# Optimization experiments

Measured on AMD Instinct MI355X. Metric: run time of the kernel, lower is better.

The kernel has to match this reference:

```python
import jax, jax.numpy as jnp
import numpy as np

N = 50000
E = 1600000
IN, OUT = 128, 64


def _gcn(h, W, b, src, dst):
    # DGL GraphConv, norm='both', weight applied first (in>out), activation=relu
    x = h @ W  # [N, OUT]
    ones = jnp.ones((src.shape[0],), dtype=h.dtype)
    deg_out = jnp.clip(jax.ops.segment_sum(ones, src, num_segments=N), 1.0)
    deg_in = jnp.clip(jax.ops.segment_sum(ones, dst, num_segments=N), 1.0)
    x = x * jax.lax.rsqrt(deg_out)[:, None]
    agg = jax.ops.segment_sum(x[src], dst, num_segments=N)  # SpMM
    agg = agg * jax.lax.rsqrt(deg_in)[:, None]
    return jax.nn.relu(agg + b)


def setup_inputs() -> dict:
    key = jax.random.key(0)
    ks = jax.random.split(key, 10)
    inp = {"h": jax.random.normal(ks[0], (N, IN), dtype=jnp.float32)}
    for i in range(3):
        inp[f"src{i}"] = jax.random.randint(ks[1 + 2 * i], (E,), 0, N, dtype=jnp.int32)
        inp[f"dst{i}"] = jax.random.randint(ks[2 + 2 * i], (E,), 0, N, dtype=jnp.int32)
        inp[f"W{i}"] = jax.random.normal(ks[7 + i], (IN, OUT), dtype=jnp.float32) * (1.0 / np.sqrt(IN))
        inp[f"b{i}"] = jnp.zeros((OUT,), dtype=jnp.float32)
    return inp


def reference(h, src0, dst0, src1, dst1, src2, dst2, W0, b0, W1, b1, W2, b2):
    e0 = _gcn(h, W0, b0, src0, dst0)
    e1 = _gcn(h, W1, b1, src1, dst1)
    e2 = _gcn(h, W2, b2, src2, dst2)
    # stack over meta-path dim then mean == average of semantic embeddings
    return (e0 + e1 + e2) / 3.0
```

## Files before the change

kernel.cpp:

```cpp
#include <hip/hip_runtime.h>

#define KDIM 128
#define NCOLS 64
#define NHCH 64
#define HW 12500
#define COARSE 512
#define NC 98
#define SFCAP 17408
#define BUCKET 64
#define NBUCK 782
#define FCAP 2816
#define NPB 85
#define PREP_HIST (3 * NHCH)
#define PREP_CNT  (3 * NPB)
#define PREP_WF   12
#define PREP_CONV 565
#define PREP_GRID (PREP_HIST + PREP_CNT + PREP_WF + PREP_CONV)

typedef __attribute__((ext_vector_type(8))) short bf16x8;
typedef __attribute__((ext_vector_type(4))) float f32x4;

struct GArgs {
  const int*   src[3];
  const int*   dst[3];
  const float* W[3];
  const float* b[3];
  int          E[3];
};

__device__ __forceinline__ unsigned short f2bf(float f) {
  unsigned u = __float_as_uint(f);
  u += 0x7FFFu + ((u >> 16) & 1u);
  return (unsigned short)(u >> 16);
}
__device__ __forceinline__ float bflo(unsigned u) { return __uint_as_float(u << 16); }
__device__ __forceinline__ float bfhi(unsigned u) { return __uint_as_float(u & 0xFFFF0000u); }

__global__ __launch_bounds__(256) void prep_kernel(
    GArgs A, const float* __restrict__ h, unsigned short* __restrict__ hb,
    unsigned short* __restrict__ Wf, unsigned* __restrict__ P8,
    int* __restrict__ tot, int total8) {
  __shared__ unsigned sbuf[HW];
  const int b = blockIdx.x;
  const int t = threadIdx.x;

  if (b < PREP_HIST) {
    const int g = b >> 6;
    const int chunk = b & 63;
    const int E = A.E[g];
    const int per_chunk = (((E + NHCH - 1) / NHCH) + 3) & ~3;
    const int* __restrict__ keys = A.src[g];
    for (int i = t; i < HW; i += 256) sbuf[i] = 0;
    __syncthreads();
    const int e0 = chunk * per_chunk;
    const int e1 = min(e0 + per_chunk, E);
    const int nn = max(e1 - e0, 0);
    const int nv = nn >> 2;
    const int4* k4p = (const int4*)&keys[e0];
    for (int v = t; v < nv; v += 256) {
      int4 k = k4p[v];
      atomicAdd(&sbuf[(unsigned)k.x >> 2], 1u << (((unsigned)k.x & 3u) * 8));
      atomicAdd(&sbuf[(unsigned)k.y >> 2], 1u << (((unsigned)k.y & 3u) * 8));
      atomicAdd(&sbuf[(unsigned)k.z >> 2], 1u << (((unsigned)k.z & 3u) * 8));
      atomicAdd(&sbuf[(unsigned)k.w >> 2], 1u << (((unsigned)k.w & 3u) * 8));
    }
    for (int e = e0 + (nv << 2) + t; e < e1; e += 256) {
      unsigned k = (unsigned)keys[e];
      atomicAdd(&sbuf[k >> 2], 1u << ((k & 3u) * 8));
    }
    __syncthreads();
    unsigned* __restrict__ dstp = P8 + (size_t)b * HW;
    for (int i = t; i < HW; i += 256) dstp[i] = sbuf[i];

  } else if (b < PREP_HIST + PREP_CNT) {
    const int bb = b - PREP_HIST;
    const int g = bb / NPB;
    const int blk = bb % NPB;
    const int E = A.E[g];
    const int per_block = (((E + NPB - 1) / NPB) + 3) & ~3;
    const int* __restrict__ dst = A.dst[g];
    int* hcnt = (int*)sbuf;
    if (t < NC) hcnt[t] = 0;
    __syncthreads();
    const int e0 = blk * per_block;
    const int e1 = min(e0 + per_block, E);
    const int nn = max(e1 - e0, 0);
    const int nv = nn >> 2;
    const int4* d4 = (const int4*)&dst[e0];
    for (int v = t; v < nv; v += 256) {
      int4 d = d4[v];
      atomicAdd(&hcnt[(unsigned)d.x >> 9], 1);
      atomicAdd(&hcnt[(unsigned)d.y >> 9], 1);
      atomicAdd(&hcnt[(unsigned)d.z >> 9], 1);
      atomicAdd(&hcnt[(unsigned)d.w >> 9], 1);
    }
    for (int e = e0 + (nv << 2) + t; e < e1; e += 256)
      atomicAdd(&hcnt[(unsigned)dst[e] >> 9], 1);
    __syncthreads();
    if (t < NC && hcnt[t]) atomicAdd(&tot[g * NC + t], hcnt[t]);

  } else if (b < PREP_HIST + PREP_CNT + PREP_WF) {
    int tid = (b - PREP_HIST - PREP_CNT) * 256 + t;
    int lane = tid & 63;
    int frag = (tid >> 6) & 15;
    int g = tid >> 10;
    int c = frag >> 2, kk = frag & 3;
    int n = lane & 15, quad = lane >> 4;
    const float* W = A.W[g];
    unsigned short v[8];
    #pragma unroll
    for (int j = 0; j < 8; ++j) {
      int k = 32 * kk + quad * 8 + j;
      v[j] = f2bf(W[k * 64 + 4 * n + c]);
    }
    uint4 u;
    u.x = (unsigned)v[0] | ((unsigned)v[1] << 16);
    u.y = (unsigned)v[2] | ((unsigned)v[3] << 16);
    u.z = (unsigned)v[4] | ((unsigned)v[5] << 16);
    u.w = (unsigned)v[6] | ((unsigned)v[7] << 16);
    ((uint4*)Wf)[tid] = u;

  } else {
    const int cb = b - (PREP_HIST + PREP_CNT + PREP_WF);
    for (int i = cb * 256 + t; i < total8; i += PREP_CONV * 256) {
      const float4* hp = (const float4*)(h + (size_t)i * 8);
      float4 f0 = hp[0];
      float4 f1 = hp[1];
      uint4 u;
      u.x = (unsigned)f2bf(f0.x) | ((unsigned)f2bf(f0.y) << 16);
      u.y = (unsigned)f2bf(f0.z) | ((unsigned)f2bf(f0.w) << 16);
      u.z = (unsigned)f2bf(f1.x) | ((unsigned)f2bf(f1.y) << 16);
      u.w = (unsigned)f2bf(f1.z) | ((unsigned)f2bf(f1.w) << 16);
      ((uint4*)hb)[i] = u;
    }
  }
}

__global__ __launch_bounds__(128) void scan_off_kernel(
    const int* __restrict__ tot, int* __restrict__ off, int* __restrict__ cursor) {
  __shared__ int sd[128];
  const int t = threadIdx.x;
  for (int g = 0; g < 3; ++g) {
    int v = (t < NC) ? tot[g * NC + t] : 0;
    sd[t] = v;
    __syncthreads();
    for (int o = 1; o < 128; o <<= 1) {
      int add = (t >= o) ? sd[t - o] : 0;
      __syncthreads();
      sd[t] += add;
      __syncthreads();
    }
    int excl = sd[t] - v;
    if (t < NC) { off[g * (NC + 1) + t] = excl; cursor[g * NC + t] = excl; }
    if (t == 0) off[g * (NC + 1) + NC] = sd[127];
    __syncthreads();
  }
}

__global__ __launch_bounds__(256) void partition_coarse_kernel(
    GArgs A, int* __restrict__ cursor, unsigned* __restrict__ P2c, int Emax) {
  __shared__ int lcnt[NC];
  __shared__ int lcur[NC];
  const int g = blockIdx.y;
  const int E = A.E[g];
  const int per_block = (((E + NPB - 1) / NPB) + 3) & ~3;
  const int* __restrict__ src = A.src[g];
  const int* __restrict__ dst = A.dst[g];
  unsigned* __restrict__ P2g = P2c + (size_t)g * Emax;
  const int t = threadIdx.x;
  if (t < NC) lcnt[t] = 0;
  __syncthreads();
  const int e0 = blockIdx.x * per_block;
  const int e1 = min(e0 + per_block, E);
  const int n = max(e1 - e0, 0);
  const int nv = n >> 2;
  const int4* d4 = (const int4*)&dst[e0];
  const int4* s4 = (const int4*)&src[e0];
  for (int v = t; v < nv; v += 256) {
    int4 d = d4[v];
    atomicAdd(&lcnt[(unsigned)d.x >> 9], 1);
    atomicAdd(&lcnt[(unsigned)d.y >> 9], 1);
    atomicAdd(&lcnt[(unsigned)d.z >> 9], 1);
    atomicAdd(&lcnt[(unsigned)d.w >> 9], 1);
  }
  for (int e = e0 + (nv << 2) + t; e < e1; e += 256)
    atomicAdd(&lcnt[(unsigned)dst[e] >> 9], 1);
  __syncthreads();
  if (t < NC) {
    int c = lcnt[t];
    lcur[t] = c ? atomicAdd(&cursor[g * NC + t], c) : 0;
  }
  __syncthreads();
  for (int v = t; v < nv; v += 256) {
    int4 d = d4[v];
    int4 s = s4[v];
    unsigned bk; int pos;
    bk = (unsigned)d.x >> 9; pos = atomicAdd(&lcur[bk], 1);
    P2g[pos] = (unsigned)s.x | (((unsigned)d.x & 511u) << 16);
    bk = (unsigned)d.y >> 9; pos = atomicAdd(&lcur[bk], 1);
    P2g[pos] = (unsigned)s.y | (((unsigned)d.y & 511u) << 16);
    bk = (unsigned)d.z >> 9; pos = atomicAdd(&lcur[bk], 1);
    P2g[pos] = (unsigned)s.z | (((unsigned)d.z & 511u) << 16);
    bk = (unsigned)d.w >> 9; pos = atomicAdd(&lcur[bk], 1);
    P2g[pos] = (unsigned)s.w | (((unsigned)d.w & 511u) << 16);
  }
  for (int e = e0 + (nv << 2) + t; e < e1; e += 256) {
    unsigned d = (unsigned)dst[e];
    unsigned bk = d >> 9;
    int pos = atomicAdd(&lcur[bk], 1);
    P2g[pos] = (unsigned)src[e] | ((d & 511u) << 16);
  }
}

__global__ __launch_bounds__(512) void sort_fine_kernel(
    const unsigned* __restrict__ P2c, const int* __restrict__ off,
    unsigned short* __restrict__ S, int* __restrict__ row_start,
    int N, int Emax) {
  __shared__ int cnt[COARSE];
  __shared__ int sd[COARSE];
  __shared__ int cur[COARSE];
  __shared__ unsigned short outl[SFCAP];
  const int c = blockIdx.x;
  const int g = blockIdx.y;
  const unsigned* __restrict__ P2g = P2c + (size_t)g * Emax;
  const int base_e = off[g * (NC + 1) + c];
  const int nloc = off[g * (NC + 1) + c + 1] - base_e;
  const int t = threadIdx.x;

  cnt[t] = 0;
  __syncthreads();
  for (int i = t; i < nloc; i += 512)
    atomicAdd(&cnt[(P2g[base_e + i] >> 16) & 511u], 1);
  __syncthreads();
  int v = cnt[t];
  sd[t] = v;
  __syncthreads();
  for (int o = 1; o < 512; o <<= 1) {
    int add = (t >= o) ? sd[t - o] : 0;
    __syncthreads();
    sd[t] += add;
    __syncthreads();
  }
  int excl = sd[t] - v;
  cur[t] = excl;
  int node = c * COARSE + t;
  if (node <= N) row_start[g * (N + 1) + node] = base_e + excl;
  __syncthreads();
  for (int i = t; i < nloc; i += 512) {
    unsigned p = P2g[base_e + i];
    int pos = atomicAdd(&cur[(p >> 16) & 511u], 1);
    if (pos < SFCAP) outl[pos] = (unsigned short)(p & 0xFFFFu);
  }
  __syncthreads();
  unsigned short* __restrict__ Sg = S + (size_t)g * Emax;
  for (int i = t; i < nloc; i += 512) Sg[base_e + i] = outl[i];
}

__global__ __launch_bounds__(512) void gemm_mfma_kernel(
    GArgs A, const unsigned short* __restrict__ hb,
    const unsigned short* __restrict__ Wf, const unsigned* __restrict__ P8,
    unsigned short* __restrict__ x, int N) {
  __shared__ unsigned ldegw[64];
  const int g = blockIdx.y;
  unsigned short* __restrict__ xg = x + (size_t)g * N * NCOLS;
  const int t = threadIdx.x;
  const int row0 = blockIdx.x * 128;

  if (t < 64) ldegw[t] = 0;
  __syncthreads();
  if (t < 256) {
    const unsigned* __restrict__ Pg = P8 + (size_t)g * NHCH * HW;
    const int widx = t >> 3;
    const int cg = t & 7;
    const int wcol = min((row0 >> 2) + widx, HW - 1);
    unsigned lo = 0, hi = 0;
    #pragma unroll
    for (int cc = 0; cc < 8; ++cc) {
      unsigned wv = Pg[(size_t)(cg * 8 + cc) * HW + wcol];
      lo += wv & 0x00FF00FFu;
      hi += (wv >> 8) & 0x00FF00FFu;
    }
    atomicAdd(&ldegw[2 * widx], lo);
    atomicAdd(&ldegw[2 * widx + 1], hi);
  }

  const int lane = t & 63;
  const int w = t >> 6;
  const int quad = lane >> 4;
  const int n = lane & 15;

  int arow = min(row0 + w * 16 + n, N - 1);
  const unsigned short* hrow = hb + (size_t)arow * KDIM + quad * 8;
  bf16x8 a0 = *(const bf16x8*)(hrow);
  bf16x8 a1 = *(const bf16x8*)(hrow + 32);
  bf16x8 a2 = *(const bf16x8*)(hrow + 64);
  bf16x8 a3 = *(const bf16x8*)(hrow + 96);

  const uint4* wfp = (const uint4*)Wf + (size_t)g * 1024 + lane;

  f32x4 acc[4];
  #pragma unroll
  for (int c = 0; c < 4; ++c) acc[c] = (f32x4)(0.f);

  __syncthreads();

  #pragma unroll
  for (int c = 0; c < 4; ++c) {
    union { uint4 u; bf16x8 v; } b0, b1, b2, b3;
    b0.u = wfp[(size_t)(c * 4 + 0) * 64];
    b1.u = wfp[(size_t)(c * 4 + 1) * 64];
    b2.u = wfp[(size_t)(c * 4 + 2) * 64];
    b3.u = wfp[(size_t)(c * 4 + 3) * 64];
    acc[c] = __builtin_amdgcn_mfma_f32_16x16x32_bf16(a0, b0.v, acc[c], 0, 0, 0);
    acc[c] = __builtin_amdgcn_mfma_f32_16x16x32_bf16(a1, b1.v, acc[c], 0, 0, 0);
    acc[c] = __builtin_amdgcn_mfma_f32_16x16x32_bf16(a2, b2.v, acc[c], 0, 0, 0);
    acc[c] = __builtin_amdgcn_mfma_f32_16x16x32_bf16(a3, b3.v, acc[c], 0, 0, 0);
  }

  const int rbase = row0 + w * 16 + quad * 4;
  #pragma unroll
  for (int r = 0; r < 4; ++r) {
    int row = rbase + r;
    if (row < N) {
      int lr = row - row0;
      float dg = (float)((ldegw[2 * (lr >> 2) + (lr & 1)] >> (((lr >> 1) & 1) * 16)) & 0xFFFFu);
      float s = rsqrtf(fmaxf(dg, 1.0f));
      uint2 o;
      o.x = (unsigned)f2bf(acc[0][r] * s) | ((unsigned)f2bf(acc[1][r] * s) << 16);
      o.y = (unsigned)f2bf(acc[2][r] * s) | ((unsigned)f2bf(acc[3][r] * s) << 16);
      *(uint2*)(xg + (size_t)row * NCOLS + 4 * n) = o;
    }
  }
}

__global__ __launch_bounds__(512) void spmm_all_kernel(
    GArgs A, const unsigned short* __restrict__ S,
    const int* __restrict__ row_start, const unsigned short* __restrict__ x,
    float* __restrict__ out, int N, int Emax) {
  __shared__ int rs[BUCKET + 1];
  __shared__ unsigned short srcs[FCAP];

  const int t = threadIdx.x;
  const int bk = blockIdx.x;
  const int dbase = bk * BUCKET;
  const int nd = min(BUCKET, N - dbase);
  const int grp = t >> 3;
  const int qe = (t & 7) * 8;

  float tot[8];
  #pragma unroll
  for (int j = 0; j < 8; ++j) tot[j] = 0.f;

  for (int g = 0; g < 3; ++g) {
    const unsigned short* __restrict__ Sg = S + (size_t)g * Emax;
    const int* __restrict__ rsg = row_start + (size_t)g * (N + 1);
    const unsigned short* __restrict__ xg = x + (size_t)g * N * NCOLS;

    __syncthreads();
    if (t <= BUCKET) rs[t] = rsg[min(dbase + t, N)];
    __syncthreads();
    const int e0 = rs[0];
    const int ne = min(rs[BUCKET] - e0, FCAP);
    for (int i = t; i < ne; i += 512) srcs[i] = Sg[e0 + i];
    __syncthreads();

    if (grp < nd) {
      int i = rs[grp] - e0;
      const int iend = min(rs[grp + 1] - e0, ne);
      const int deg = iend - i;
      float acc[8];
      #pragma unroll
      for (int j = 0; j < 8; ++j) acc[j] = 0.f;
      for (; i + 3 < iend; i += 4) {
        int sa = srcs[i + 0];
        int sb = srcs[i + 1];
        int sc = srcs[i + 2];
        int sdd = srcs[i + 3];
        uint4 ua = *(const uint4*)&xg[(size_t)sa * NCOLS + qe];
        uint4 ub = *(const uint4*)&xg[(size_t)sb * NCOLS + qe];
        uint4 uc = *(const uint4*)&xg[(size_t)sc * NCOLS + qe];
        uint4 ud = *(const uint4*)&xg[(size_t)sdd * NCOLS + qe];
        acc[0] += bflo(ua.x) + bflo(ub.x) + bflo(uc.x) + bflo(ud.x);
        acc[1] += bfhi(ua.x) + bfhi(ub.x) + bfhi(uc.x) + bfhi(ud.x);
        acc[2] += bflo(ua.y) + bflo(ub.y) + bflo(uc.y) + bflo(ud.y);
        acc[3] += bfhi(ua.y) + bfhi(ub.y) + bfhi(uc.y) + bfhi(ud.y);
        acc[4] += bflo(ua.z) + bflo(ub.z) + bflo(uc.z) + bflo(ud.z);
        acc[5] += bfhi(ua.z) + bfhi(ub.z) + bfhi(uc.z) + bfhi(ud.z);
        acc[6] += bflo(ua.w) + bflo(ub.w) + bflo(uc.w) + bflo(ud.w);
        acc[7] += bfhi(ua.w) + bfhi(ub.w) + bfhi(uc.w) + bfhi(ud.w);
      }
      for (; i < iend; ++i) {
        int s = srcs[i];
        uint4 u = *(const uint4*)&xg[(size_t)s * NCOLS + qe];
        acc[0] += bflo(u.x); acc[1] += bfhi(u.x);
        acc[2] += bflo(u.y); acc[3] += bfhi(u.y);
        acc[4] += bflo(u.z); acc[5] += bfhi(u.z);
        acc[6] += bflo(u.w); acc[7] += bfhi(u.w);
      }
      float sc2 = rsqrtf(fmaxf((float)deg, 1.0f));
      const float* bg = A.b[g] + qe;
      #pragma unroll
      for (int j = 0; j < 8; ++j)
        tot[j] += fmaxf(fmaf(acc[j], sc2, bg[j]), 0.f) * (1.0f / 3.0f);
    }
  }

  if (grp < nd) {
    float* op = &out[(size_t)(dbase + grp) * NCOLS + qe];
    *(float4*)&op[0] = make_float4(tot[0], tot[1], tot[2], tot[3]);
    *(float4*)&op[4] = make_float4(tot[4], tot[5], tot[6], tot[7]);
  }
}

extern "C" void kernel_launch(void* const* d_in, const int* in_sizes, int n_in,
                              void* d_out, int out_size, void* d_ws, size_t ws_size,
                              hipStream_t stream) {
  const float* h = (const float*)d_in[0];
  const int N = in_sizes[0] / KDIM;
  float* out = (float*)d_out;

  GArgs A;
  int Emax = 0;
  for (int g = 0; g < 3; ++g) {
    A.src[g] = (const int*)  d_in[1 + g * 4];
    A.dst[g] = (const int*)  d_in[2 + g * 4];
    A.W[g]   = (const float*)d_in[3 + g * 4];
    A.b[g]   = (const float*)d_in[4 + g * 4];
    A.E[g]   = in_sizes[1 + g * 4];
    if (A.E[g] > Emax) Emax = A.E[g];
  }

  char* w = (char*)d_ws;
  unsigned short* x = (unsigned short*)w;
  char* w2 = w + (size_t)3 * N * NCOLS * sizeof(unsigned short);
  unsigned short* hb = (unsigned short*)w2;
  char* w3 = w2 + (size_t)N * KDIM * sizeof(unsigned short);
  unsigned* P2c = (unsigned*)w3;
  char* w4 = w3 + (size_t)3 * Emax * sizeof(unsigned);
  unsigned* P8 = (unsigned*)w4;
  char* w5 = w4 + (size_t)3 * NHCH * HW * sizeof(unsigned);
  unsigned short* S = (unsigned short*)w5;
  char* w6 = w5 + (size_t)3 * Emax * sizeof(unsigned short);
  unsigned short* Wf = (unsigned short*)w6;
  char* w7 = w6 + (size_t)3 * 16 * 64 * 8 * sizeof(unsigned short);
  int* row_start = (int*)w7;
  char* w8 = w7 + (size_t)3 * (N + 1) * sizeof(int);
  int* tot    = (int*)w8;
  int* off    = tot + 3 * NC;
  int* cursor = off + 3 * (NC + 1);

  hipMemsetAsync(tot, 0, 3 * NC * sizeof(int), stream);
  const int total8 = N * KDIM / 8;
  prep_kernel<<<PREP_GRID, 256, 0, stream>>>(A, h, hb, Wf, P8, tot, total8);
  scan_off_kernel<<<1, 128, 0, stream>>>(tot, off, cursor);
  partition_coarse_kernel<<<dim3(NPB, 3), 256, 0, stream>>>(A, cursor, P2c, Emax);
  sort_fine_kernel<<<dim3(NC, 3), 512, 0, stream>>>(P2c, off, S, row_start, N, Emax);
  gemm_mfma_kernel<<<dim3((N + 127) / 128, 3), 512, 0, stream>>>(A, hb, Wf, P8, x, N);
  spmm_all_kernel<<<NBUCK, 512, 0, stream>>>(A, S, row_start, x, out, N, Emax);
}
```

Before: 268.7 us.

## Replace two-level bucket sort with global-atomic degree counting and direct scatter

Drops the shared-memory packed histograms and the coarse-partition plus fine-sort pipeline. Per-node in and out degrees are now counted with global atomics, row_start comes from a per-chunk scan, and edges are scattered straight into CSR with global atomic cursors. That scatter is fused into one launch with the MFMA GEMM so the two can overlap. This removes several launches and passes over the edge data, at the cost of heavy contended global atomics and a nondeterministic order of edges within each row.

```diff
diff --git a/kernel.cpp b/kernel.cpp
--- a/kernel.cpp
+++ b/kernel.cpp
@@ -2,20 +2,18 @@
 
 #define KDIM 128
 #define NCOLS 64
-#define NHCH 64
-#define HW 12500
-#define COARSE 512
-#define NC 98
-#define SFCAP 17408
 #define BUCKET 64
 #define NBUCK 782
 #define FCAP 2816
 #define NPB 85
-#define PREP_HIST (3 * NHCH)
-#define PREP_CNT  (3 * NPB)
-#define PREP_WF   12
-#define PREP_CONV 565
-#define PREP_GRID (PREP_HIST + PREP_CNT + PREP_WF + PREP_CONV)
+#define PREP_DEG (3 * NPB)
+#define PREP_WF  12
+#define PREP_CONV 757
+#define PREP_GRID (PREP_DEG + PREP_WF + PREP_CONV)
+#define PG_SCAT (3 * NPB)
+#define PG_GEMM_PER 391
+#define PG_GEMM (3 * PG_GEMM_PER)
+#define PG_GRID (PG_SCAT + PG_GEMM)
 
 typedef __attribute__((ext_vector_type(8))) short bf16x8;
 typedef __attribute__((ext_vector_type(4))) float f32x4;
@@ -38,69 +36,41 @@
 
 __global__ __launch_bounds__(256) void prep_kernel(
     GArgs A, const float* __restrict__ h, unsigned short* __restrict__ hb,
-    unsigned short* __restrict__ Wf, unsigned* __restrict__ P8,
-    int* __restrict__ tot, int total8) {
-  __shared__ unsigned sbuf[HW];
+    unsigned short* __restrict__ Wf, int* __restrict__ deg_out,
+    int* __restrict__ deg_in, int N, int total8) {
   const int b = blockIdx.x;
   const int t = threadIdx.x;
 
-  if (b < PREP_HIST) {
-    const int g = b >> 6;
-    const int chunk = b & 63;
-    const int E = A.E[g];
-    const int per_chunk = (((E + NHCH - 1) / NHCH) + 3) & ~3;
-    const int* __restrict__ keys = A.src[g];
-    for (int i = t; i < HW; i += 256) sbuf[i] = 0;
-    __syncthreads();
-    const int e0 = chunk * per_chunk;
-    const int e1 = min(e0 + per_chunk, E);
-    const int nn = max(e1 - e0, 0);
-    const int nv = nn >> 2;
-    const int4* k4p = (const int4*)&keys[e0];
-    for (int v = t; v < nv; v += 256) {
-      int4 k = k4p[v];
-      atomicAdd(&sbuf[(unsigned)k.x >> 2], 1u << (((unsigned)k.x & 3u) * 8));
-      atomicAdd(&sbuf[(unsigned)k.y >> 2], 1u << (((unsigned)k.y & 3u) * 8));
-      atomicAdd(&sbuf[(unsigned)k.z >> 2], 1u << (((unsigned)k.z & 3u) * 8));
-      atomicAdd(&sbuf[(unsigned)k.w >> 2], 1u << (((unsigned)k.w & 3u) * 8));
-    }
-    for (int e = e0 + (nv << 2) + t; e < e1; e += 256) {
-      unsigned k = (unsigned)keys[e];
-      atomicAdd(&sbuf[k >> 2], 1u << ((k & 3u) * 8));
-    }
-    __syncthreads();
-    unsigned* __restrict__ dstp = P8 + (size_t)b * HW;
-    for (int i = t; i < HW; i += 256) dstp[i] = sbuf[i];
-
-  } else if (b < PREP_HIST + PREP_CNT) {
-    const int bb = b - PREP_HIST;
-    const int g = bb / NPB;
-    const int blk = bb % NPB;
+  if (b < PREP_DEG) {
+    const int g = b / NPB;
+    const int blk = b % NPB;
     const int E = A.E[g];
     const int per_block = (((E + NPB - 1) / NPB) + 3) & ~3;
+    const int* __restrict__ src = A.src[g];
     const int* __restrict__ dst = A.dst[g];
-    int* hcnt = (int*)sbuf;
-    if (t < NC) hcnt[t] = 0;
-    __syncthreads();
+    int* __restrict__ dout = deg_out + (size_t)g * N;
+    int* __restrict__ din  = deg_in  + (size_t)g * N;
     const int e0 = blk * per_block;
     const int e1 = min(e0 + per_block, E);
     const int nn = max(e1 - e0, 0);
     const int nv = nn >> 2;
+    const int4* s4 = (const int4*)&src[e0];
     const int4* d4 = (const int4*)&dst[e0];
     for (int v = t; v < nv; v += 256) {
+      int4 s = s4[v];
       int4 d = d4[v];
-      atomicAdd(&hcnt[(unsigned)d.x >> 9], 1);
-      atomicAdd(&hcnt[(unsigned)d.y >> 9], 1);
-      atomicAdd(&hcnt[(unsigned)d.z >> 9], 1);
-      atomicAdd(&hcnt[(unsigned)d.w >> 9], 1);
-    }
-    for (int e = e0 + (nv << 2) + t; e < e1; e += 256)
-      atomicAdd(&hcnt[(unsigned)dst[e] >> 9], 1);
-    __syncthreads();
-    if (t < NC && hcnt[t]) atomicAdd(&tot[g * NC + t], hcnt[t]);
-
-  } else if (b < PREP_HIST + PREP_CNT + PREP_WF) {
-    int tid = (b - PREP_HIST - PREP_CNT) * 256 + t;
+      atomicAdd(&dout[s.x], 1); atomicAdd(&dout[s.y], 1);
+      atomicAdd(&dout[s.z], 1); atomicAdd(&dout[s.w], 1);
+      atomicAdd(&din[d.x], 1);  atomicAdd(&din[d.y], 1);
+      atomicAdd(&din[d.z], 1);  atomicAdd(&din[d.w], 1);
+    }
+    for (int e = e0 + (nv << 2) + t; e < e1; e += 256) {
+      atomicAdd(&dout[src[e]], 1);
+      atomicAdd(&din[dst[e]], 1);
+    }
+
+  } else if (b < PREP_DEG + PREP_WF) {
+    int tid = (b - PREP_DEG) * 256 + t;
     int lane = tid & 63;
     int frag = (tid >> 6) & 15;
     int g = tid >> 10;
@@ -121,7 +91,7 @@
     ((uint4*)Wf)[tid] = u;
 
   } else {
-    const int cb = b - (PREP_HIST + PREP_CNT + PREP_WF);
+    const int cb = b - (PREP_DEG + PREP_WF);
     for (int i = cb * 256 + t; i < total8; i += PREP_CONV * 256) {
       const float4* hp = (const float4*)(h + (size_t)i * 8);
       float4 f0 = hp[0];
@@ -136,103 +106,30 @@
   }
 }
 
-__global__ __launch_bounds__(128) void scan_off_kernel(
-    const int* __restrict__ tot, int* __restrict__ off, int* __restrict__ cursor) {
-  __shared__ int sd[128];
+__global__ __launch_bounds__(512) void scan_rs_kernel(
+    const int* __restrict__ deg_in, int* __restrict__ row_start,
+    int* __restrict__ cursor, int N) {
+  __shared__ int sd[512];
+  __shared__ int sbase;
+  const int g = blockIdx.y;
+  const int c = blockIdx.x;
   const int t = threadIdx.x;
-  for (int g = 0; g < 3; ++g) {
-    int v = (t < NC) ? tot[g * NC + t] : 0;
-    sd[t] = v;
-    __syncthreads();
-    for (int o = 1; o < 128; o <<= 1) {
-      int add = (t >= o) ? sd[t - o] : 0;
-      __syncthreads();
-      sd[t] += add;
-      __syncthreads();
-    }
-    int excl = sd[t] - v;
-    if (t < NC) { off[g * (NC + 1) + t] = excl; cursor[g * NC + t] = excl; }
-    if (t == 0) off[g * (NC + 1) + NC] = sd[127];
-    __syncthreads();
-  }
-}
-
-__global__ __launch_bounds__(256) void partition_coarse_kernel(
-    GArgs A, int* __restrict__ cursor, unsigned* __restrict__ P2c, int Emax) {
-  __shared__ int lcnt[NC];
-  __shared__ int lcur[NC];
-  const int g = blockIdx.y;
-  const int E = A.E[g];
-  const int per_block = (((E + NPB - 1) / NPB) + 3) & ~3;
-  const int* __restrict__ src = A.src[g];
-  const int* __restrict__ dst = A.dst[g];
-  unsigned* __restrict__ P2g = P2c + (size_t)g * Emax;
-  const int t = threadIdx.x;
-  if (t < NC) lcnt[t] = 0;
+  const int* __restrict__ dg = deg_in + (size_t)g * N;
+
+  int acc = 0;
+  const int c512 = c * 512;
+  for (int i = t; i < c512; i += 512) acc += dg[i];
+  sd[t] = acc;
   __syncthreads();
-  const int e0 = blockIdx.x * per_block;
-  const int e1 = min(e0 + per_block, E);
-  const int n = max(e1 - e0, 0);
-  const int nv = n >> 2;
-  const int4* d4 = (const int4*)&dst[e0];
-  const int4* s4 = (const int4*)&src[e0];
-  for (int v = t; v < nv; v += 256) {
-    int4 d = d4[v];
-    atomicAdd(&lcnt[(unsigned)d.x >> 9], 1);
-    atomicAdd(&lcnt[(unsigned)d.y >> 9], 1);
-    atomicAdd(&lcnt[(unsigned)d.z >> 9], 1);
-    atomicAdd(&lcnt[(unsigned)d.w >> 9], 1);
-  }
-  for (int e = e0 + (nv << 2) + t; e < e1; e += 256)
-    atomicAdd(&lcnt[(unsigned)dst[e] >> 9], 1);
+  for (int o = 256; o > 0; o >>= 1) {
+    if (t < o) sd[t] += sd[t + o];
+    __syncthreads();
+  }
+  if (t == 0) sbase = sd[0];
   __syncthreads();
-  if (t < NC) {
-    int c = lcnt[t];
-    lcur[t] = c ? atomicAdd(&cursor[g * NC + t], c) : 0;
-  }
-  __syncthreads();
-  for (int v = t; v < nv; v += 256) {
-    int4 d = d4[v];
-    int4 s = s4[v];
-    unsigned bk; int pos;
-    bk = (unsigned)d.x >> 9; pos = atomicAdd(&lcur[bk], 1);
-    P2g[pos] = (unsigned)s.x | (((unsigned)d.x & 511u) << 16);
-    bk = (unsigned)d.y >> 9; pos = atomicAdd(&lcur[bk], 1);
-    P2g[pos] = (unsigned)s.y | (((unsigned)d.y & 511u) << 16);
-    bk = (unsigned)d.z >> 9; pos = atomicAdd(&lcur[bk], 1);
-    P2g[pos] = (unsigned)s.z | (((unsigned)d.z & 511u) << 16);
-    bk = (unsigned)d.w >> 9; pos = atomicAdd(&lcur[bk], 1);
-    P2g[pos] = (unsigned)s.w | (((unsigned)d.w & 511u) << 16);
-  }
-  for (int e = e0 + (nv << 2) + t; e < e1; e += 256) {
-    unsigned d = (unsigned)dst[e];
-    unsigned bk = d >> 9;
-    int pos = atomicAdd(&lcur[bk], 1);
-    P2g[pos] = (unsigned)src[e] | ((d & 511u) << 16);
-  }
-}
-
-__global__ __launch_bounds__(512) void sort_fine_kernel(
-    const unsigned* __restrict__ P2c, const int* __restrict__ off,
-    unsigned short* __restrict__ S, int* __restrict__ row_start,
-    int N, int Emax) {
-  __shared__ int cnt[COARSE];
-  __shared__ int sd[COARSE];
-  __shared__ int cur[COARSE];
-  __shared__ unsigned short outl[SFCAP];
-  const int c = blockIdx.x;
-  const int g = blockIdx.y;
-  const unsigned* __restrict__ P2g = P2c + (size_t)g * Emax;
-  const int base_e = off[g * (NC + 1) + c];
-  const int nloc = off[g * (NC + 1) + c + 1] - base_e;
-  const int t = threadIdx.x;
-
-  cnt[t] = 0;
-  __syncthreads();
-  for (int i = t; i < nloc; i += 512)
-    atomicAdd(&cnt[(P2g[base_e + i] >> 16) & 511u], 1);
-  __syncthreads();
-  int v = cnt[t];
+
+  const int idx = c512 + t;
+  int v = (idx < N) ? dg[idx] : 0;
   sd[t] = v;
   __syncthreads();
   for (int o = 1; o < 512; o <<= 1) {
@@ -241,94 +138,106 @@
     sd[t] += add;
     __syncthreads();
   }
-  int excl = sd[t] - v;
-  cur[t] = excl;
-  int node = c * COARSE + t;
-  if (node <= N) row_start[g * (N + 1) + node] = base_e + excl;
-  __syncthreads();
-  for (int i = t; i < nloc; i += 512) {
-    unsigned p = P2g[base_e + i];
-    int pos = atomicAdd(&cur[(p >> 16) & 511u], 1);
-    if (pos < SFCAP) outl[pos] = (unsigned short)(p & 0xFFFFu);
-  }
-  __syncthreads();
-  unsigned short* __restrict__ Sg = S + (size_t)g * Emax;
-  for (int i = t; i < nloc; i += 512) Sg[base_e + i] = outl[i];
-}
-
-__global__ __launch_bounds__(512) void gemm_mfma_kernel(
+  int excl = sbase + sd[t] - v;
+  if (idx < N) {
+    row_start[(size_t)g * (N + 1) + idx] = excl;
+    cursor[(size_t)g * N + idx] = excl;
+  } else if (idx == N) {
+    row_start[(size_t)g * (N + 1) + N] = excl;
+  }
+}
+
+__global__ __launch_bounds__(512) void pg_kernel(
     GArgs A, const unsigned short* __restrict__ hb,
-    const unsigned short* __restrict__ Wf, const unsigned* __restrict__ P8,
-    unsigned short* __restrict__ x, int N) {
-  __shared__ unsigned ldegw[64];
-  const int g = blockIdx.y;
-  unsigned short* __restrict__ xg = x + (size_t)g * N * NCOLS;
+    const unsigned short* __restrict__ Wf, const int* __restrict__ deg_out,
+    int* __restrict__ cursor, unsigned short* __restrict__ S,
+    unsigned short* __restrict__ x, int N, int Emax) {
+  const int b = blockIdx.x;
   const int t = threadIdx.x;
-  const int row0 = blockIdx.x * 128;
-
-  if (t < 64) ldegw[t] = 0;
-  __syncthreads();
-  if (t < 256) {
-    const unsigned* __restrict__ Pg = P8 + (size_t)g * NHCH * HW;
-    const int widx = t >> 3;
-    const int cg = t & 7;
-    const int wcol = min((row0 >> 2) + widx, HW - 1);
-    unsigned lo = 0, hi = 0;
+
+  if (b < PG_SCAT) {
+    const int g = b / NPB;
+    const int blk = b % NPB;
+    const int E = A.E[g];
+    const int per_block = (((E + NPB - 1) / NPB) + 3) & ~3;
+    const int* __restrict__ src = A.src[g];
+    const int* __restrict__ dst = A.dst[g];
+    int* __restrict__ cur = cursor + (size_t)g * N;
+    unsigned short* __restrict__ Sg = S + (size_t)g * Emax;
+    const int e0 = blk * per_block;
+    const int e1 = min(e0 + per_block, E);
+    const int nn = max(e1 - e0, 0);
+    const int nv = nn >> 2;
+    const int4* s4 = (const int4*)&src[e0];
+    const int4* d4 = (const int4*)&dst[e0];
+    for (int v = t; v < nv; v += 512) {
+      int4 s = s4[v];
+      int4 d = d4[v];
+      int p0 = atomicAdd(&cur[d.x], 1);
+      int p1 = atomicAdd(&cur[d.y], 1);
+      int p2 = atomicAdd(&cur[d.z], 1);
+      int p3 = atomicAdd(&cur[d.w], 1);
+      Sg[p0] = (unsigned short)s.x;
+      Sg[p1] = (unsigned short)s.y;
+      Sg[p2] = (unsigned short)s.z;
+      Sg[p3] = (unsigned short)s.w;
+    }
+    for (int e = e0 + (nv << 2) + t; e < e1; e += 512) {
+      int p = atomicAdd(&cur[dst[e]], 1);
+      Sg[p] = (unsigned short)src[e];
+    }
+
+  } else {
+    const int gb = b - PG_SCAT;
+    const int g = gb / PG_GEMM_PER;
+    const int blk = gb % PG_GEMM_PER;
+    const int row0 = blk * 128;
+    unsigned short* __restrict__ xg = x + (size_t)g * N * NCOLS;
+    const int* __restrict__ degg = deg_out + (size_t)g * N;
+
+    const int lane = t & 63;
+    const int w = t >> 6;
+    const int quad = lane >> 4;
+    const int n = lane & 15;
+
+    int arow = min(row0 + w * 16 + n, N - 1);
+    const unsigned short* hrow = hb + (size_t)arow * KDIM + quad * 8;
+    bf16x8 a0 = *(const bf16x8*)(hrow);
+    bf16x8 a1 = *(const bf16x8*)(hrow + 32);
+    bf16x8 a2 = *(const bf16x8*)(hrow + 64);
+    bf16x8 a3 = *(const bf16x8*)(hrow + 96);
+
+    const uint4* wfp = (const uint4*)Wf + (size_t)g * 1024 + lane;
+
+    f32x4 acc[4];
     #pragma unroll
-    for (int cc = 0; cc < 8; ++cc) {
-      unsigned wv = Pg[(size_t)(cg * 8 + cc) * HW + wcol];
-      lo += wv & 0x00FF00FFu;
-      hi += (wv >> 8) & 0x00FF00FFu;
-    }
-    atomicAdd(&ldegw[2 * widx], lo);
-    atomicAdd(&ldegw[2 * widx + 1], hi);
-  }
-
-  const int lane = t & 63;
-  const int w = t >> 6;
-  const int quad = lane >> 4;
-  const int n = lane & 15;
-
-  int arow = min(row0 + w * 16 + n, N - 1);
-  const unsigned short* hrow = hb + (size_t)arow * KDIM + quad * 8;
-  bf16x8 a0 = *(const bf16x8*)(hrow);
-  bf16x8 a1 = *(const bf16x8*)(hrow + 32);
-  bf16x8 a2 = *(const bf16x8*)(hrow + 64);
-  bf16x8 a3 = *(const bf16x8*)(hrow + 96);
-
-  const uint4* wfp = (const uint4*)Wf + (size_t)g * 1024 + lane;
-
-  f32x4 acc[4];
-  #pragma unroll
-  for (int c = 0; c < 4; ++c) acc[c] = (f32x4)(0.f);
-
-  __syncthreads();
-
-  #pragma unroll
-  for (int c = 0; c < 4; ++c) {
-    union { uint4 u; bf16x8 v; } b0, b1, b2, b3;
-    b0.u = wfp[(size_t)(c * 4 + 0) * 64];
-    b1.u = wfp[(size_t)(c * 4 + 1) * 64];
-    b2.u = wfp[(size_t)(c * 4 + 2) * 64];
-    b3.u = wfp[(size_t)(c * 4 + 3) * 64];
-    acc[c] = __builtin_amdgcn_mfma_f32_16x16x32_bf16(a0, b0.v, acc[c], 0, 0, 0);
-    acc[c] = __builtin_amdgcn_mfma_f32_16x16x32_bf16(a1, b1.v, acc[c], 0, 0, 0);
-    acc[c] = __builtin_amdgcn_mfma_f32_16x16x32_bf16(a2, b2.v, acc[c], 0, 0, 0);
-    acc[c] = __builtin_amdgcn_mfma_f32_16x16x32_bf16(a3, b3.v, acc[c], 0, 0, 0);
-  }
-
-  const int rbase = row0 + w * 16 + quad * 4;
-  #pragma unroll
-  for (int r = 0; r < 4; ++r) {
-    int row = rbase + r;
-    if (row < N) {
-      int lr = row - row0;
-      float dg = (float)((ldegw[2 * (lr >> 2) + (lr & 1)] >> (((lr >> 1) & 1) * 16)) & 0xFFFFu);
-      float s = rsqrtf(fmaxf(dg, 1.0f));
-      uint2 o;
-      o.x = (unsigned)f2bf(acc[0][r] * s) | ((unsigned)f2bf(acc[1][r] * s) << 16);
-      o.y = (unsigned)f2bf(acc[2][r] * s) | ((unsigned)f2bf(acc[3][r] * s) << 16);
-      *(uint2*)(xg + (size_t)row * NCOLS + 4 * n) = o;
+    for (int c = 0; c < 4; ++c) acc[c] = (f32x4)(0.f);
+
+    #pragma unroll
+    for (int c = 0; c < 4; ++c) {
+      union { uint4 u; bf16x8 v; } b0, b1, b2, b3;
+      b0.u = wfp[(size_t)(c * 4 + 0) * 64];
+      b1.u = wfp[(size_t)(c * 4 + 1) * 64];
+      b2.u = wfp[(size_t)(c * 4 + 2) * 64];
+      b3.u = wfp[(size_t)(c * 4 + 3) * 64];
+      acc[c] = __builtin_amdgcn_mfma_f32_16x16x32_bf16(a0, b0.v, acc[c], 0, 0, 0);
+      acc[c] = __builtin_amdgcn_mfma_f32_16x16x32_bf16(a1, b1.v, acc[c], 0, 0, 0);
+      acc[c] = __builtin_amdgcn_mfma_f32_16x16x32_bf16(a2, b2.v, acc[c], 0, 0, 0);
+      acc[c] = __builtin_amdgcn_mfma_f32_16x16x32_bf16(a3, b3.v, acc[c], 0, 0, 0);
+    }
+
+    const int rbase = row0 + w * 16 + quad * 4;
+    #pragma unroll
+    for (int r = 0; r < 4; ++r) {
+      int row = rbase + r;
+      if (row < N) {
+        float dg = (float)degg[row];
+        float s = rsqrtf(fmaxf(dg, 1.0f));
+        uint2 o;
+        o.x = (unsigned)f2bf(acc[0][r] * s) | ((unsigned)f2bf(acc[1][r] * s) << 16);
+        o.y = (unsigned)f2bf(acc[2][r] * s) | ((unsigned)f2bf(acc[3][r] * s) << 16);
+        *(uint2*)(xg + (size_t)row * NCOLS + 4 * n) = o;
+      }
     }
   }
 }
@@ -435,26 +344,19 @@
   char* w2 = w + (size_t)3 * N * NCOLS * sizeof(unsigned short);
   unsigned short* hb = (unsigned short*)w2;
   char* w3 = w2 + (size_t)N * KDIM * sizeof(unsigned short);
-  unsigned* P2c = (unsigned*)w3;
-  char* w4 = w3 + (size_t)3 * Emax * sizeof(unsigned);
-  unsigned* P8 = (unsigned*)w4;
-  char* w5 = w4 + (size_t)3 * NHCH * HW * sizeof(unsigned);
-  unsigned short* S = (unsigned short*)w5;
-  char* w6 = w5 + (size_t)3 * Emax * sizeof(unsigned short);
-  unsigned short* Wf = (unsigned short*)w6;
-  char* w7 = w6 + (size_t)3 * 16 * 64 * 8 * sizeof(unsigned short);
-  int* row_start = (int*)w7;
-  char* w8 = w7 + (size_t)3 * (N + 1) * sizeof(int);
-  int* tot    = (int*)w8;
-  int* off    = tot + 3 * NC;
-  int* cursor = off + 3 * (NC + 1);
-
-  hipMemsetAsync(tot, 0, 3 * NC * sizeof(int), stream);
+  unsigned short* S = (unsigned short*)w3;
+  char* w4 = w3 + (size_t)3 * Emax * sizeof(unsigned short);
+  unsigned short* Wf = (unsigned short*)w4;
+  char* w5 = w4 + (size_t)3 * 16 * 64 * 8 * sizeof(unsigned short);
+  int* deg_out = (int*)w5;
+  int* deg_in  = deg_out + (size_t)3 * N;
+  int* cursor  = deg_in + (size_t)3 * N;
+  int* row_start = cursor + (size_t)3 * N;
+
+  hipMemsetAsync(deg_out, 0, (size_t)2 * 3 * N * sizeof(int), stream);
   const int total8 = N * KDIM / 8;
-  prep_kernel<<<PREP_GRID, 256, 0, stream>>>(A, h, hb, Wf, P8, tot, total8);
-  scan_off_kernel<<<1, 128, 0, stream>>>(tot, off, cursor);
-  partition_coarse_kernel<<<dim3(NPB, 3), 256, 0, stream>>>(A, cursor, P2c, Emax);
-  sort_fine_kernel<<<dim3(NC, 3), 512, 0, stream>>>(P2c, off, S, row_start, N, Emax);
-  gemm_mfma_kernel<<<dim3((N + 127) / 128, 3), 512, 0, stream>>>(A, hb, Wf, P8, x, N);
+  prep_kernel<<<PREP_GRID, 256, 0, stream>>>(A, h, hb, Wf, deg_out, deg_in, N, total8);
+  scan_rs_kernel<<<dim3(98, 3), 512, 0, stream>>>(deg_in, row_start, cursor, N);
+  pg_kernel<<<PG_GRID, 512, 0, stream>>>(A, hb, Wf, deg_out, cursor, S, x, N, Emax);
   spmm_all_kernel<<<NBUCK, 512, 0, stream>>>(A, S, row_start, x, out, N, Emax);
 }
```

Result: slower. 956.2 us (+255.8%).

## Partition edges directly into 64-node buckets and sort locally inside SpMM

Applied to the files above, without the earlier changes.

Replaces the two-level sort (coarse 512-node partition followed by a separate fine-sort kernel that writes CSR row_start and a compact source array) with a single partition into 782 buckets of 64 destination nodes. Each SpMM block then loads its bucket's packed edges into shared memory, builds a per-node histogram, scans it with a wavefront shuffle and scatters sources locally before aggregating. This removes one kernel launch and one full pass over the edge array, but adds LDS counting-sort work to each SpMM block and uses wider histograms with more global atomics in the prep and partition stages.

```diff
diff --git a/kernel.cpp b/kernel.cpp
--- a/kernel.cpp
+++ b/kernel.cpp
@@ -4,11 +4,8 @@
 #define NCOLS 64
 #define NHCH 64
 #define HW 12500
-#define COARSE 512
-#define NC 98
-#define SFCAP 17408
 #define BUCKET 64
-#define NBUCK 782
+#define NB7 782
 #define FCAP 2816
 #define NPB 85
 #define PREP_HIST (3 * NHCH)
@@ -80,7 +77,7 @@
     const int per_block = (((E + NPB - 1) / NPB) + 3) & ~3;
     const int* __restrict__ dst = A.dst[g];
     int* hcnt = (int*)sbuf;
-    if (t < NC) hcnt[t] = 0;
+    for (int i = t; i < NB7; i += 256) hcnt[i] = 0;
     __syncthreads();
     const int e0 = blk * per_block;
     const int e1 = min(e0 + per_block, E);
@@ -89,15 +86,16 @@
     const int4* d4 = (const int4*)&dst[e0];
     for (int v = t; v < nv; v += 256) {
       int4 d = d4[v];
-      atomicAdd(&hcnt[(unsigned)d.x >> 9], 1);
-      atomicAdd(&hcnt[(unsigned)d.y >> 9], 1);
-      atomicAdd(&hcnt[(unsigned)d.z >> 9], 1);
-      atomicAdd(&hcnt[(unsigned)d.w >> 9], 1);
+      atomicAdd(&hcnt[(unsigned)d.x >> 6], 1);
+      atomicAdd(&hcnt[(unsigned)d.y >> 6], 1);
+      atomicAdd(&hcnt[(unsigned)d.z >> 6], 1);
+      atomicAdd(&hcnt[(unsigned)d.w >> 6], 1);
     }
     for (int e = e0 + (nv << 2) + t; e < e1; e += 256)
-      atomicAdd(&hcnt[(unsigned)dst[e] >> 9], 1);
-    __syncthreads();
-    if (t < NC && hcnt[t]) atomicAdd(&tot[g * NC + t], hcnt[t]);
+      atomicAdd(&hcnt[(unsigned)dst[e] >> 6], 1);
+    __syncthreads();
+    for (int i = t; i < NB7; i += 256)
+      if (hcnt[i]) atomicAdd(&tot[g * NB7 + i], hcnt[i]);
 
   } else if (b < PREP_HIST + PREP_CNT + PREP_WF) {
     int tid = (b - PREP_HIST - PREP_CNT) * 256 + t;
@@ -136,39 +134,46 @@
   }
 }
 
-__global__ __launch_bounds__(128) void scan_off_kernel(
+__global__ __launch_bounds__(512) void scan782_kernel(
     const int* __restrict__ tot, int* __restrict__ off, int* __restrict__ cursor) {
-  __shared__ int sd[128];
+  __shared__ int sd[512];
+  const int g = blockIdx.x;
   const int t = threadIdx.x;
-  for (int g = 0; g < 3; ++g) {
-    int v = (t < NC) ? tot[g * NC + t] : 0;
+  int base = 0;
+  for (int c0 = 0; c0 < NB7; c0 += 512) {
+    int idx = c0 + t;
+    int v = (idx < NB7) ? tot[g * NB7 + idx] : 0;
     sd[t] = v;
     __syncthreads();
-    for (int o = 1; o < 128; o <<= 1) {
+    for (int o = 1; o < 512; o <<= 1) {
       int add = (t >= o) ? sd[t - o] : 0;
       __syncthreads();
       sd[t] += add;
       __syncthreads();
     }
-    int excl = sd[t] - v;
-    if (t < NC) { off[g * (NC + 1) + t] = excl; cursor[g * NC + t] = excl; }
-    if (t == 0) off[g * (NC + 1) + NC] = sd[127];
-    __syncthreads();
-  }
-}
-
-__global__ __launch_bounds__(256) void partition_coarse_kernel(
-    GArgs A, int* __restrict__ cursor, unsigned* __restrict__ P2c, int Emax) {
-  __shared__ int lcnt[NC];
-  __shared__ int lcur[NC];
+    int excl = base + sd[t] - v;
+    if (idx < NB7) {
+      off[g * (NB7 + 1) + idx] = excl;
+      cursor[g * NB7 + idx] = excl;
+    }
+    base += sd[511];
+    __syncthreads();
+  }
+  if (t == 0) off[g * (NB7 + 1) + NB7] = base;
+}
+
+__global__ __launch_bounds__(256) void partition_fine_kernel(
+    GArgs A, int* __restrict__ cursor, unsigned* __restrict__ P2, int Emax) {
+  __shared__ int lcnt[NB7];
+  __shared__ int lcur[NB7];
   const int g = blockIdx.y;
   const int E = A.E[g];
   const int per_block = (((E + NPB - 1) / NPB) + 3) & ~3;
   const int* __restrict__ src = A.src[g];
   const int* __restrict__ dst = A.dst[g];
-  unsigned* __restrict__ P2g = P2c + (size_t)g * Emax;
+  unsigned* __restrict__ P2g = P2 + (size_t)g * Emax;
   const int t = threadIdx.x;
-  if (t < NC) lcnt[t] = 0;
+  for (int i = t; i < NB7; i += 256) lcnt[i] = 0;
   __syncthreads();
   const int e0 = blockIdx.x * per_block;
   const int e1 = min(e0 + per_block, E);
@@ -178,82 +183,38 @@
   const int4* s4 = (const int4*)&src[e0];
   for (int v = t; v < nv; v += 256) {
     int4 d = d4[v];
-    atomicAdd(&lcnt[(unsigned)d.x >> 9], 1);
-    atomicAdd(&lcnt[(unsigned)d.y >> 9], 1);
-    atomicAdd(&lcnt[(unsigned)d.z >> 9], 1);
-    atomicAdd(&lcnt[(unsigned)d.w >> 9], 1);
+    atomicAdd(&lcnt[(unsigned)d.x >> 6], 1);
+    atomicAdd(&lcnt[(unsigned)d.y >> 6], 1);
+    atomicAdd(&lcnt[(unsigned)d.z >> 6], 1);
+    atomicAdd(&lcnt[(unsigned)d.w >> 6], 1);
   }
   for (int e = e0 + (nv << 2) + t; e < e1; e += 256)
-    atomicAdd(&lcnt[(unsigned)dst[e] >> 9], 1);
+    atomicAdd(&lcnt[(unsigned)dst[e] >> 6], 1);
   __syncthreads();
-  if (t < NC) {
-    int c = lcnt[t];
-    lcur[t] = c ? atomicAdd(&cursor[g * NC + t], c) : 0;
+  for (int i = t; i < NB7; i += 256) {
+    int c = lcnt[i];
+    lcur[i] = c ? atomicAdd(&cursor[g * NB7 + i], c) : 0;
   }
   __syncthreads();
   for (int v = t; v < nv; v += 256) {
     int4 d = d4[v];
     int4 s = s4[v];
     unsigned bk; int pos;
-    bk = (unsigned)d.x >> 9; pos = atomicAdd(&lcur[bk], 1);
-    P2g[pos] = (unsigned)s.x | (((unsigned)d.x & 511u) << 16);
-    bk = (unsigned)d.y >> 9; pos = atomicAdd(&lcur[bk], 1);
-    P2g[pos] = (unsigned)s.y | (((unsigned)d.y & 511u) << 16);
-    bk = (unsigned)d.z >> 9; pos = atomicAdd(&lcur[bk], 1);
-    P2g[pos] = (unsigned)s.z | (((unsigned)d.z & 511u) << 16);
-    bk = (unsigned)d.w >> 9; pos = atomicAdd(&lcur[bk], 1);
-    P2g[pos] = (unsigned)s.w | (((unsigned)d.w & 511u) << 16);
+    bk = (unsigned)d.x >> 6; pos = atomicAdd(&lcur[bk], 1);
+    P2g[pos] = (unsigned)s.x | (((unsigned)d.x & 63u) << 16);
+    bk = (unsigned)d.y >> 6; pos = atomicAdd(&lcur[bk], 1);
+    P2g[pos] = (unsigned)s.y | (((unsigned)d.y & 63u) << 16);
+    bk = (unsigned)d.z >> 6; pos = atomicAdd(&lcur[bk], 1);
+    P2g[pos] = (unsigned)s.z | (((unsigned)d.z & 63u) << 16);
+    bk = (unsigned)d.w >> 6; pos = atomicAdd(&lcur[bk], 1);
+    P2g[pos] = (unsigned)s.w | (((unsigned)d.w & 63u) << 16);
   }
   for (int e = e0 + (nv << 2) + t; e < e1; e += 256) {
     unsigned d = (unsigned)dst[e];
-    unsigned bk = d >> 9;
+    unsigned bk = d >> 6;
     int pos = atomicAdd(&lcur[bk], 1);
-    P2g[pos] = (unsigned)src[e] | ((d & 511u) << 16);
-  }
-}
-
-__global__ __launch_bounds__(512) void sort_fine_kernel(
-    const unsigned* __restrict__ P2c, const int* __restrict__ off,
-    unsigned short* __restrict__ S, int* __restrict__ row_start,
-    int N, int Emax) {
-  __shared__ int cnt[COARSE];
-  __shared__ int sd[COARSE];
-  __shared__ int cur[COARSE];
-  __shared__ unsigned short outl[SFCAP];
-  const int c = blockIdx.x;
-  const int g = blockIdx.y;
-  const unsigned* __restrict__ P2g = P2c + (size_t)g * Emax;
-  const int base_e = off[g * (NC + 1) + c];
-  const int nloc = off[g * (NC + 1) + c + 1] - base_e;
-  const int t = threadIdx.x;
-
-  cnt[t] = 0;
-  __syncthreads();
-  for (int i = t; i < nloc; i += 512)
-    atomicAdd(&cnt[(P2g[base_e + i] >> 16) & 511u], 1);
-  __syncthreads();
-  int v = cnt[t];
-  sd[t] = v;
-  __syncthreads();
-  for (int o = 1; o < 512; o <<= 1) {
-    int add = (t >= o) ? sd[t - o] : 0;
-    __syncthreads();
-    sd[t] += add;
-    __syncthreads();
-  }
-  int excl = sd[t] - v;
-  cur[t] = excl;
-  int node = c * COARSE + t;
-  if (node <= N) row_start[g * (N + 1) + node] = base_e + excl;
-  __syncthreads();
-  for (int i = t; i < nloc; i += 512) {
-    unsigned p = P2g[base_e + i];
-    int pos = atomicAdd(&cur[(p >> 16) & 511u], 1);
-    if (pos < SFCAP) outl[pos] = (unsigned short)(p & 0xFFFFu);
-  }
-  __syncthreads();
-  unsigned short* __restrict__ Sg = S + (size_t)g * Emax;
-  for (int i = t; i < nloc; i += 512) Sg[base_e + i] = outl[i];
+    P2g[pos] = (unsigned)src[e] | ((d & 63u) << 16);
+  }
 }
 
 __global__ __launch_bounds__(512) void gemm_mfma_kernel(
@@ -334,11 +295,14 @@
 }
 
 __global__ __launch_bounds__(512) void spmm_all_kernel(
-    GArgs A, const unsigned short* __restrict__ S,
-    const int* __restrict__ row_start, const unsigned short* __restrict__ x,
-    float* __restrict__ out, int N, int Emax) {
-  __shared__ int rs[BUCKET + 1];
+    GArgs A, const unsigned* __restrict__ P2, const int* __restrict__ off,
+    const unsigned short* __restrict__ x, float* __restrict__ out,
+    int N, int Emax) {
+  __shared__ unsigned eb[FCAP];
   __shared__ unsigned short srcs[FCAP];
+  __shared__ int cnt[BUCKET];
+  __shared__ int cur[BUCKET];
+  __shared__ int rsx[BUCKET + 1];
 
   const int t = threadIdx.x;
   const int bk = blockIdx.x;
@@ -352,21 +316,46 @@
   for (int j = 0; j < 8; ++j) tot[j] = 0.f;
 
   for (int g = 0; g < 3; ++g) {
-    const unsigned short* __restrict__ Sg = S + (size_t)g * Emax;
-    const int* __restrict__ rsg = row_start + (size_t)g * (N + 1);
+    const unsigned* __restrict__ P2g = P2 + (size_t)g * Emax;
     const unsigned short* __restrict__ xg = x + (size_t)g * N * NCOLS;
 
     __syncthreads();
-    if (t <= BUCKET) rs[t] = rsg[min(dbase + t, N)];
-    __syncthreads();
-    const int e0 = rs[0];
-    const int ne = min(rs[BUCKET] - e0, FCAP);
-    for (int i = t; i < ne; i += 512) srcs[i] = Sg[e0 + i];
+    if (t < BUCKET) cnt[t] = 0;
+    __syncthreads();
+
+    const int e0 = off[g * (NB7 + 1) + bk];
+    const int ne = min(off[g * (NB7 + 1) + bk + 1] - e0, FCAP);
+    for (int i = t; i < ne; i += 512) {
+      unsigned e = P2g[e0 + i];
+      eb[i] = e;
+      atomicAdd(&cnt[e >> 16], 1);
+    }
+    __syncthreads();
+
+    if (t < BUCKET) {
+      int v = cnt[t];
+      int incl = v;
+      #pragma unroll
+      for (int o = 1; o < 64; o <<= 1) {
+        int u = __shfl_up(incl, o, 64);
+        if (t >= o) incl += u;
+      }
+      rsx[t + 1] = incl;
+      cur[t] = incl - v;
+      if (t == 0) rsx[0] = 0;
+    }
+    __syncthreads();
+
+    for (int i = t; i < ne; i += 512) {
+      unsigned e = eb[i];
+      int pos = atomicAdd(&cur[e >> 16], 1);
+      srcs[pos] = (unsigned short)(e & 0xFFFFu);
+    }
     __syncthreads();
 
     if (grp < nd) {
-      int i = rs[grp] - e0;
-      const int iend = min(rs[grp + 1] - e0, ne);
+      int i = rsx[grp];
+      const int iend = rsx[grp + 1];
       const int deg = iend - i;
       float acc[8];
       #pragma unroll
@@ -435,26 +424,21 @@
   char* w2 = w + (size_t)3 * N * NCOLS * sizeof(unsigned short);
   unsigned short* hb = (unsigned short*)w2;
   char* w3 = w2 + (size_t)N * KDIM * sizeof(unsigned short);
-  unsigned* P2c = (unsigned*)w3;
+  unsigned* P2 = (unsigned*)w3;
   char* w4 = w3 + (size_t)3 * Emax * sizeof(unsigned);
   unsigned* P8 = (unsigned*)w4;
   char* w5 = w4 + (size_t)3 * NHCH * HW * sizeof(unsigned);
-  unsigned short* S = (unsigned short*)w5;
-  char* w6 = w5 + (size_t)3 * Emax * sizeof(unsigned short);
-  unsigned short* Wf = (unsigned short*)w6;
-  char* w7 = w6 + (size_t)3 * 16 * 64 * 8 * sizeof(unsigned short);
-  int* row_start = (int*)w7;
-  char* w8 = w7 + (size_t)3 * (N + 1) * sizeof(int);
-  int* tot    = (int*)w8;
-  int* off    = tot + 3 * NC;
-  int* cursor = off + 3 * (NC + 1);
-
-  hipMemsetAsync(tot, 0, 3 * NC * sizeof(int), stream);
+  unsigned short* Wf = (unsigned short*)w5;
+  char* w6 = w5 + (size_t)3 * 16 * 64 * 8 * sizeof(unsigned short);
+  int* tot    = (int*)w6;
+  int* cursor = tot + 3 * NB7;
+  int* off    = cursor + 3 * NB7;
+
+  hipMemsetAsync(tot, 0, 3 * NB7 * sizeof(int), stream);
   const int total8 = N * KDIM / 8;
   prep_kernel<<<PREP_GRID, 256, 0, stream>>>(A, h, hb, Wf, P8, tot, total8);
-  scan_off_kernel<<<1, 128, 0, stream>>>(tot, off, cursor);
-  partition_coarse_kernel<<<dim3(NPB, 3), 256, 0, stream>>>(A, cursor, P2c, Emax);
-  sort_fine_kernel<<<dim3(NC, 3), 512, 0, stream>>>(P2c, off, S, row_start, N, Emax);
+  scan782_kernel<<<3, 512, 0, stream>>>(tot, off, cursor);
+  partition_fine_kernel<<<dim3(NPB, 3), 256, 0, stream>>>(A, cursor, P2, Emax);
   gemm_mfma_kernel<<<dim3((N + 127) / 128, 3), 512, 0, stream>>>(A, hb, Wf, P8, x, N);
-  spmm_all_kernel<<<NBUCK, 512, 0, stream>>>(A, S, row_start, x, out, N, Emax);
-}
+  spmm_all_kernel<<<NB7, 512, 0, stream>>>(A, P2, off, x, out, N, Emax);
+}
```

Measured after the change: 263.9 us. About the same (-1.8%).
